# Kernel tuning notes

Measured on AMD Instinct MI355X. Metric: run time of the kernel, lower is better.

Reference implementation:

```python
import jax, jax.numpy as jnp
import numpy as np

HS = 256      # hidden_size
HD = 256      # hidden_dim
B, L, S = 256, 400, 512
N = B * L
E = N * 4
NEG_SLOPE = 0.2


def setup_inputs() -> dict:
    key = jax.random.key(0)
    ks = iter(jax.random.split(key, 48))
    def rn(shape, scale=0.05):
        return jax.random.normal(next(ks), shape, jnp.float32) * scale
    inp = {}
    inp['emb'] = jax.random.normal(next(ks), (N, 640), jnp.float32)
    inp['x_tokens'] = jax.random.randint(next(ks), (N,), 0, 6, jnp.int32)
    inp['edge_src'] = jax.random.randint(next(ks), (E,), 0, N, jnp.int32)
    inp['edge_dst'] = jax.random.randint(next(ks), (E,), 0, N, jnp.int32)
    inp['batch_ids'] = (jnp.arange(N, dtype=jnp.int32) // L)
    inp['pos_ids'] = (jnp.arange(N, dtype=jnp.int32) % L)
    inp['mask'] = (jnp.arange(S)[None, :] < L).astype(jnp.float32) * jnp.ones((B, 1), jnp.float32)
    # parameters
    inp['emb_table'] = rn((6, HS))
    inp['W_e2g'] = rn((640, HS)); inp['b_e2g'] = jnp.zeros((HS,), jnp.float32)
    # GAT layers: (in, heads*out), att_src/att_dst [heads, out], bias [out]
    inp['W1'] = rn((HS, 4 * HD)); inp['asrc1'] = rn((4, HD)); inp['adst1'] = rn((4, HD)); inp['b1'] = jnp.zeros((HD,), jnp.float32)
    inp['W2'] = rn((HD, 4 * HD)); inp['asrc2'] = rn((4, HD)); inp['adst2'] = rn((4, HD)); inp['b2'] = jnp.zeros((HD,), jnp.float32)
    inp['W3'] = rn((HD, 1 * HS)); inp['asrc3'] = rn((1, HS)); inp['adst3'] = rn((1, HS)); inp['b3'] = jnp.zeros((HS,), jnp.float32)
    inp['W_le'] = rn((640, HS)); inp['b_le'] = jnp.zeros((HS,), jnp.float32)
    # CNN conv kernels: OIH layout [out=128, in=256, k]
    inp['k7'] = rn((HS // 2, HS, 7)); inp['cb7'] = jnp.zeros((HS // 2,), jnp.float32)
    inp['k11'] = rn((HS // 2, HS, 11)); inp['cb11'] = jnp.zeros((HS // 2,), jnp.float32)
    inp['k15'] = rn((HS // 2, HS, 15)); inp['cb15'] = jnp.zeros((HS // 2,), jnp.float32)
    inp['Wl1'] = rn((HS // 2, 512)); inp['bl1'] = jnp.zeros((512,), jnp.float32)
    inp['Wl2'] = rn((512, HS)); inp['bl2'] = jnp.zeros((HS,), jnp.float32)
    return inp


def _gat(x, src, dst, W, a_src, a_dst, b, heads, out_dim):
    # PyG GATConv, concat=False, eval (no dropout), with self-loops.
    n = x.shape[0]
    h = (x @ W).reshape(n, heads, out_dim)             # [N,H,C]
    al_s = (h * a_src[None]).sum(-1)                   # [N,H]
    al_d = (h * a_dst[None]).sum(-1)                   # [N,H]
    e = al_s[src] + al_d[dst]                          # [E,H]
    e = jnp.where(e > 0, e, NEG_SLOPE * e)             # leaky_relu(0.2)
    m = jax.ops.segment_max(e, dst, num_segments=n)
    m = jnp.where(jnp.isfinite(m), m, 0.0)
    ex = jnp.exp(e - m[dst])
    denom = jax.ops.segment_sum(ex, dst, num_segments=n) + 1e-16
    alpha = ex / denom[dst]                            # [E,H]
    out = jax.ops.segment_sum(alpha[:, :, None] * h[src], dst, num_segments=n)
    return out.mean(axis=1) + b                        # concat=False -> mean over heads


def _conv1d(x, w, b, pad):
    # x: [B,C,S], w: [O,I,k]
    y = jax.lax.conv_general_dilated(x, w, (1,), [(pad, pad)],
                                     dimension_numbers=('NCH', 'OIH', 'NCH'))
    return y + b[None, :, None]


def reference(emb, x_tokens, edge_src, edge_dst, batch_ids, pos_ids, mask,
              emb_table, W_e2g, b_e2g,
              W1, asrc1, adst1, b1, W2, asrc2, adst2, b2, W3, asrc3, adst3, b3,
              W_le, b_le, k7, cb7, k11, cb11, k15, cb15, Wl1, bl1, Wl2, bl2):
    n = emb.shape[0]
    # self-loops (PyG GATConv default)
    loops = jnp.arange(n, dtype=edge_src.dtype)
    src = jnp.concatenate([edge_src, loops])
    dst = jnp.concatenate([edge_dst, loops])

    x_r = emb_table[x_tokens]                          # [N,HS]
    x_g = jax.nn.relu(emb @ W_e2g + b_e2g)             # [N,HS]
    x = jax.nn.relu(_gat(x_g, src, dst, W1, asrc1, adst1, b1, 4, HD))
    x = jax.nn.relu(_gat(x, src, dst, W2, asrc2, adst2, b2, 4, HD))
    x = jax.nn.relu(_gat(x, src, dst, W3, asrc3, adst3, b3, 1, HS))

    emb_l = jax.nn.relu(emb @ W_le + b_le)             # [N,HS]

    # ragged -> padded [B,S,HS] via scatter (vectorized form of the python loop)
    zeros = jnp.zeros((mask.shape[0], S, HS), jnp.float32)
    out_r = zeros.at[batch_ids, pos_ids].set((x_r + emb_l) / 2)

    # CNN (eval: dropout = identity)
    xc = out_r.transpose(0, 2, 1)                      # [B,HS,S]
    x1 = _conv1d(xc, k7, cb7, 3)
    x2 = _conv1d(xc, k11, cb11, 5)
    x3 = _conv1d(xc, k15, cb15, 7)
    xc = ((x1 + x2 + x3) / 3).transpose(0, 2, 1)       # [B,S,128]
    xc = jax.nn.relu(xc @ Wl1 + bl1) @ Wl2 + bl2       # [B,S,HS]

    emb_seq = (xc * mask[:, :, None]).mean(axis=1)     # [B,HS]
    return emb_seq
```

## Files before the change

### kernel.cpp

```cpp
#include <hip/hip_runtime.h>

#define NNODES 102400
#define NBATCH 256
#define LSEQ   400
#define SPAD   416
#define HS     256
#define KDIM   640
#define OC     128
#define NTAP   15
#define H1     512

typedef __attribute__((ext_vector_type(8))) short short8;
typedef __attribute__((ext_vector_type(4))) float floatx4;

__device__ inline unsigned short f2bf(float f) {
    unsigned u = __builtin_bit_cast(unsigned, f);
    unsigned r = (u + 0x7FFFu + ((u >> 16) & 1u)) >> 16;
    return (unsigned short)r;
}

__device__ inline void gld_lds16(const void* g, void* l) {
    __builtin_amdgcn_global_load_lds(
        (const __attribute__((address_space(1))) unsigned int*)g,
        (__attribute__((address_space(3))) unsigned int*)l, 16, 0, 0);
}

__global__ __launch_bounds__(256) void combine_pack(
    const float* __restrict__ k7, const float* __restrict__ k11,
    const float* __restrict__ k15, const float* __restrict__ cb7,
    const float* __restrict__ cb11, const float* __restrict__ cb15,
    unsigned short* __restrict__ Wpk, float* __restrict__ bc)
{
    int idx = blockIdx.x * 256 + threadIdx.x;
    if (idx < NTAP * HS * OC) {
        int oc = idx & (OC - 1);
        int ic = (idx >> 7) & (HS - 1);
        int d  = idx / (OC * HS);
        float w = k15[(oc * HS + ic) * 15 + d];
        int t11 = d - 2;
        if (t11 >= 0 && t11 < 11) w += k11[(oc * HS + ic) * 11 + t11];
        int t7 = d - 4;
        if (t7 >= 0 && t7 < 7)   w += k7[(oc * HS + ic) * 7 + t7];
        w *= (1.0f / 3.0f);
        int kc = ic >> 6, ks = (ic >> 5) & 1, q = (ic >> 3) & 3, j = ic & 7;
        int nt = oc >> 4, n = oc & 15;
        int pidx = ((((d * 4 + kc) * 2 + ks) * 8 + nt) * 64 + (q * 16 + n)) * 8 + j;
        Wpk[pidx] = f2bf(w);
    }
    if (idx < OC) bc[idx] = (cb7[idx] + cb11[idx] + cb15[idx]) * (1.0f / 3.0f);
}

__global__ __launch_bounds__(256) void pack_Wle(
    const float* __restrict__ W, unsigned short* __restrict__ P)
{
    int idx = blockIdx.x * 256 + threadIdx.x;
    int k = idx >> 8, col = idx & 255;
    int t = k >> 6, ks = (k >> 5) & 1, q = (k >> 3) & 3, j = k & 7;
    int nt = col >> 4, n = col & 15;
    int pidx = (((t * 2 + ks) * 16 + nt) * 64 + (q * 16 + n)) * 8 + j;
    P[pidx] = f2bf(W[k * 256 + col]);
}

__global__ __launch_bounds__(256) void pack_Wl1(
    const float* __restrict__ W, unsigned short* __restrict__ P)
{
    int idx = blockIdx.x * 256 + threadIdx.x;
    int k = idx >> 9, col = idx & 511;
    int ks = k >> 5, q = (k >> 3) & 3, j = k & 7;
    int jb = col >> 7, nhnt = (col >> 4) & 7, n = col & 15;
    int pidx = jb * 16384 + ((ks * 8 + nhnt) * 64 + (q * 16 + n)) * 8 + j;
    P[pidx] = f2bf(W[k * 512 + col]);
}

__global__ __launch_bounds__(256) void zero_pads(unsigned short* __restrict__ seq)
{
    int idx = blockIdx.x * 256 + threadIdx.x;
    int b = idx >> 9, within = idx & 511;
    int rowi = within >> 5, c = within & 31;
    int srow = rowi < 8 ? rowi : 400 + rowi;
    ((uint4*)seq)[((size_t)b * SPAD + srow) * 32 + c] = make_uint4(0u, 0u, 0u, 0u);
}

union GemmSm {
    struct { unsigned short As[64][72]; unsigned short Bsh[16384]; } s;
    unsigned short Cs[64][264];
};

__global__ __launch_bounds__(256) void gemm_emb(
    const float* __restrict__ emb, const int* __restrict__ x_tokens,
    const float* __restrict__ emb_table,
    const unsigned short* __restrict__ Wle_pk, const float* __restrict__ b_le,
    unsigned short* __restrict__ seq)
{
    __shared__ __align__(16) GemmSm g;
    int row0 = blockIdx.x * 64;
    int tid = threadIdx.x;
    int w = tid >> 6, lane = tid & 63;
    int q = lane >> 4, m = lane & 15;
    int mh = w >> 1, nh = w & 1;

    int ar = tid >> 2;
    int ac = (tid & 3) * 16;

    floatx4 acc[2][8] = {};
    const uint4* wp = (const uint4*)Wle_pk;

    for (int t = 0; t < 10; t++) {
        __syncthreads();
        {
            const float4* src = (const float4*)&emb[(size_t)(row0 + ar) * KDIM + t * 64 + ac];
            #pragma unroll
            for (int u = 0; u < 4; u++) {
                float4 f = src[u];
                ushort4 h;
                h.x = f2bf(f.x); h.y = f2bf(f.y); h.z = f2bf(f.z); h.w = f2bf(f.w);
                *(ushort4*)&g.s.As[ar][ac + u * 4] = h;
            }
        }
        #pragma unroll
        for (int i = 0; i < 8; i++) {
            gld_lds16(wp + (size_t)t * 2048 + i * 256 + tid,
                      &g.s.Bsh[(size_t)(i * 256 + w * 64) * 8]);
        }
        __syncthreads();

        #pragma unroll
        for (int ks = 0; ks < 2; ks++) {
            short8 a0 = *(const short8*)&g.s.As[mh * 32 + m][ks * 32 + q * 8];
            short8 a1 = *(const short8*)&g.s.As[mh * 32 + 16 + m][ks * 32 + q * 8];
            #pragma unroll
            for (int nt = 0; nt < 8; nt++) {
                short8 bf = *(const short8*)&g.s.Bsh[(size_t)((ks * 16 + nh * 8 + nt) * 64 + lane) * 8];
                acc[0][nt] = __builtin_amdgcn_mfma_f32_16x16x32_bf16(a0, bf, acc[0][nt], 0, 0, 0);
                acc[1][nt] = __builtin_amdgcn_mfma_f32_16x16x32_bf16(a1, bf, acc[1][nt], 0, 0, 0);
            }
        }
    }

    __syncthreads();
    #pragma unroll
    for (int nt = 0; nt < 8; nt++) {
        int col = nh * 128 + nt * 16 + m;
        float blv = b_le[col];
        #pragma unroll
        for (int mt = 0; mt < 2; mt++) {
            #pragma unroll
            for (int r = 0; r < 4; r++) {
                int row = mh * 32 + mt * 16 + q * 4 + r;
                int tok = x_tokens[row0 + row];
                float v = acc[mt][nt][r] + blv;
                v = v > 0.f ? v : 0.f;
                g.Cs[row][col] = f2bf(0.5f * (v + emb_table[tok * HS + col]));
            }
        }
    }
    __syncthreads();
    #pragma unroll
    for (int rr = 0; rr < 16; rr++) {
        int node = row0 + w * 16 + rr;
        int b = node / LSEQ;
        int p = node - b * LSEQ;
        ushort4 val = *(const ushort4*)&g.Cs[w * 16 + rr][lane * 4];
        *(ushort4*)&seq[((size_t)b * SPAD + (p + 8)) * HS + lane * 4] = val;
    }
}

union ConvSm {
    unsigned short As[78][264];
    float red[64 * 132];
};

__device__ __forceinline__ void conv_load_B(
    const short8* __restrict__ wb, int c, int kh, int nh, int lane, short8 bf[8])
{
    int d = c >> 1, kc = kh * 2 + (c & 1);
    const short8* bp = wb + (size_t)(d * 4 + kc) * 1024 + nh * 256 + lane;
    #pragma unroll
    for (int ks = 0; ks < 2; ks++)
        #pragma unroll
        for (int nt = 0; nt < 4; nt++)
            bf[ks * 4 + nt] = bp[(ks * 8 + nt) * 64];
}

__device__ __forceinline__ void conv_mfma_chunk(
    const unsigned short (*As)[264], floatx4 acc[4][4],
    const short8 bf[8], int c, int kh, int m, int q)
{
    int d = c >> 1, kc = kh * 2 + (c & 1);
    #pragma unroll
    for (int ks = 0; ks < 2; ks++) {
        #pragma unroll
        for (int mt = 0; mt < 4; mt++) {
            short8 a = *(const short8*)&As[mt * 16 + m + d][kc * 64 + ks * 32 + q * 8];
            #pragma unroll
            for (int nt = 0; nt < 4; nt++)
                acc[mt][nt] = __builtin_amdgcn_mfma_f32_16x16x32_bf16(a, bf[ks * 4 + nt], acc[mt][nt], 0, 0, 0);
        }
    }
}

__global__ __launch_bounds__(256, 3) void conv_mfma(
    const unsigned short* __restrict__ seq, const unsigned short* __restrict__ Wpk,
    const float* __restrict__ bc, unsigned short* __restrict__ convout)
{
    __shared__ __align__(16) ConvSm sm;

    int b  = blockIdx.y;
    int s0 = blockIdx.x * 64;
    int tid = threadIdx.x;
    int w = tid >> 6, lane = tid & 63;
    int q = lane >> 4, m = lane & 15;
    int nh = w >> 1, kh = w & 1;

    const short8* wb = (const short8*)Wpk;
    short8 bufA[8], bufB[8];
    conv_load_B(wb, 0, kh, nh, lane, bufA);

    {
        const uint4* sp = (const uint4*)(seq + ((size_t)b * SPAD + s0 + 1) * HS);
        #pragma unroll
        for (int pass = 0; pass < 10; pass++) {
            int idx = pass * 256 + tid;
            if (idx < 2496) {
                int r = idx >> 5, c = idx & 31;
                uint4 v = make_uint4(0u, 0u, 0u, 0u);
                if (s0 + 1 + r < SPAD) v = sp[r * 32 + c];
                *(uint4*)&sm.As[r][c * 8] = v;
            }
        }
    }
    __syncthreads();

    floatx4 acc[4][4] = {};

    for (int c = 0; c < 30; c += 2) {
        conv_load_B(wb, c + 1, kh, nh, lane, bufB);
        conv_mfma_chunk(sm.As, acc, bufA, c, kh, m, q);
        if (c + 2 < 30) conv_load_B(wb, c + 2, kh, nh, lane, bufA);
        conv_mfma_chunk(sm.As, acc, bufB, c + 1, kh, m, q);
    }

    __syncthreads();
    if (kh == 1) {
        #pragma unroll
        for (int mt = 0; mt < 4; mt++)
            #pragma unroll
            for (int nt = 0; nt < 4; nt++)
                #pragma unroll
                for (int r = 0; r < 4; r++)
                    sm.red[(mt * 16 + q * 4 + r) * 132 + nh * 64 + nt * 16 + m] = acc[mt][nt][r];
    }
    __syncthreads();
    if (kh == 0) {
        #pragma unroll
        for (int mt = 0; mt < 4; mt++)
            #pragma unroll
            for (int nt = 0; nt < 4; nt++)
                #pragma unroll
                for (int r = 0; r < 4; r++) {
                    int idx = (mt * 16 + q * 4 + r) * 132 + nh * 64 + nt * 16 + m;
                    sm.red[idx] += acc[mt][nt][r];
                }
    }
    __syncthreads();
    float b0 = bc[lane * 2], b1 = bc[lane * 2 + 1];
    #pragma unroll
    for (int rr = 0; rr < 16; rr++) {
        int row = w * 16 + rr;
        int s = s0 + row;
        if (s < LSEQ) {
            float2 v = *(const float2*)&sm.red[row * 132 + lane * 2];
            unsigned u = (unsigned)f2bf(v.x + b0) | ((unsigned)f2bf(v.y + b1) << 16);
            *(unsigned*)&convout[((size_t)b * LSEQ + s) * OC + lane * 2] = u;
        }
    }
}

__global__ __launch_bounds__(256) void mlp1_mfma(
    const unsigned short* __restrict__ convout, const unsigned short* __restrict__ Wl1_pk,
    const float* __restrict__ bl1, float* __restrict__ A_acc)
{
    __shared__ unsigned short As[64][136];
    __shared__ unsigned short Bsh[16384];
    int b  = blockIdx.z;
    int s0 = blockIdx.y * 64;
    int jb = blockIdx.x;
    int tid = threadIdx.x;
    int w = tid >> 6, lane = tid & 63;
    int q = lane >> 4, m = lane & 15;
    int mh = w >> 1, nh = w & 1;

    {
        int r = tid >> 2;
        int c = (tid & 3) * 32;
        const uint4* src = (const uint4*)&convout[((size_t)b * LSEQ + s0 + r) * OC + c];
        bool ok = (s0 + r) < LSEQ;
        #pragma unroll
        for (int u = 0; u < 4; u++) {
            uint4 v = make_uint4(0u, 0u, 0u, 0u);
            if (ok) v = src[u];
            *(uint4*)&As[r][c + u * 8] = v;
        }
    }
    {
        const uint4* wp = (const uint4*)(Wl1_pk + (size_t)jb * 16384);
        #pragma unroll
        for (int i = 0; i < 8; i++) {
            gld_lds16(wp + i * 256 + tid, &Bsh[(size_t)(i * 256 + w * 64) * 8]);
        }
    }
    __syncthreads();

    floatx4 acc[2][4] = {};
    #pragma unroll
    for (int ks = 0; ks < 4; ks++) {
        short8 a0 = *(const short8*)&As[mh * 32 + m][ks * 32 + q * 8];
        short8 a1 = *(const short8*)&As[mh * 32 + 16 + m][ks * 32 + q * 8];
        #pragma unroll
        for (int nt = 0; nt < 4; nt++) {
            short8 bf = *(const short8*)&Bsh[(size_t)((ks * 8 + nh * 4 + nt) * 64 + lane) * 8];
            acc[0][nt] = __builtin_amdgcn_mfma_f32_16x16x32_bf16(a0, bf, acc[0][nt], 0, 0, 0);
            acc[1][nt] = __builtin_amdgcn_mfma_f32_16x16x32_bf16(a1, bf, acc[1][nt], 0, 0, 0);
        }
    }

    #pragma unroll
    for (int nt = 0; nt < 4; nt++) {
        int j = jb * 128 + nh * 64 + nt * 16 + m;
        float blv = bl1[j];
        float vsum = 0.f;
        #pragma unroll
        for (int mt = 0; mt < 2; mt++) {
            int sbase = s0 + mh * 32 + mt * 16 + q * 4;
            #pragma unroll
            for (int r = 0; r < 4; r++) {
                if (sbase + r < LSEQ) {
                    float v = acc[mt][nt][r] + blv;
                    vsum += v > 0.f ? v : 0.f;
                }
            }
        }
        vsum += __shfl_xor(vsum, 16, 64);
        vsum += __shfl_xor(vsum, 32, 64);
        if (q == 0) atomicAdd(&A_acc[(size_t)b * H1 + j], vsum);
    }
}

__global__ __launch_bounds__(256) void final_out(
    const float* __restrict__ A_acc, const float* __restrict__ Wl2,
    const float* __restrict__ bl2, float* __restrict__ out)
{
    __shared__ float a[H1];
    int b = blockIdx.x, tid = threadIdx.x;
    a[tid] = A_acc[(size_t)b * H1 + tid];
    a[tid + 256] = A_acc[(size_t)b * H1 + tid + 256];
    __syncthreads();
    float acc = 0.f;
    #pragma unroll 8
    for (int k = 0; k < H1; k++)
        acc += a[k] * Wl2[(size_t)k * HS + tid];
    out[(size_t)b * HS + tid] = acc * (1.0f / 512.0f) + bl2[tid] * (400.0f / 512.0f);
}

extern "C" void kernel_launch(void* const* d_in, const int* in_sizes, int n_in,
                              void* d_out, int out_size, void* d_ws, size_t ws_size,
                              hipStream_t stream)
{
    const float* emb       = (const float*)d_in[0];
    const int*   x_tokens  = (const int*)d_in[1];
    const float* emb_table = (const float*)d_in[7];
    const float* W_le = (const float*)d_in[22];
    const float* b_le = (const float*)d_in[23];
    const float* k7   = (const float*)d_in[24];
    const float* cb7  = (const float*)d_in[25];
    const float* k11  = (const float*)d_in[26];
    const float* cb11 = (const float*)d_in[27];
    const float* k15  = (const float*)d_in[28];
    const float* cb15 = (const float*)d_in[29];
    const float* Wl1  = (const float*)d_in[30];
    const float* bl1  = (const float*)d_in[31];
    const float* Wl2  = (const float*)d_in[32];
    const float* bl2  = (const float*)d_in[33];
    float* out = (float*)d_out;

    char* p = (char*)d_ws;
    unsigned short* seqb = (unsigned short*)p;       p += (size_t)NBATCH * SPAD * HS * 2;
    unsigned short* convout = (unsigned short*)p;    p += (size_t)NBATCH * LSEQ * OC * 2;
    unsigned short* Wpk = (unsigned short*)p;        p += (size_t)NTAP * HS * OC * 2;
    unsigned short* Wle_pk = (unsigned short*)p;     p += (size_t)KDIM * HS * 2;
    unsigned short* Wl1_pk = (unsigned short*)p;     p += (size_t)OC * H1 * 2;
    float* bcv = (float*)p;                          p += 512;
    float* A_acc = (float*)p;                        p += (size_t)NBATCH * H1 * 4;

    hipMemsetAsync(A_acc, 0, (size_t)NBATCH * H1 * sizeof(float), stream);

    zero_pads<<<dim3(NBATCH * 512 / 256), 256, 0, stream>>>(seqb);
    combine_pack<<<dim3((NTAP * HS * OC + 255) / 256), 256, 0, stream>>>(
        k7, k11, k15, cb7, cb11, cb15, Wpk, bcv);
    pack_Wle<<<dim3(KDIM * HS / 256), 256, 0, stream>>>(W_le, Wle_pk);
    pack_Wl1<<<dim3(OC * H1 / 256), 256, 0, stream>>>(Wl1, Wl1_pk);
    gemm_emb<<<dim3(NNODES / 64), 256, 0, stream>>>(
        emb, x_tokens, emb_table, Wle_pk, b_le, seqb);
    conv_mfma<<<dim3(7, NBATCH), 256, 0, stream>>>(seqb, Wpk, bcv, convout);
    mlp1_mfma<<<dim3(4, 7, NBATCH), 256, 0, stream>>>(convout, Wl1_pk, bl1, A_acc);
    final_out<<<NBATCH, 256, 0, stream>>>(A_acc, Wl2, bl2, out);
}
```

Baseline: 679.4 us.

## Fuse conv and first MLP into one kernel, retile to 80 rows, merge setup kernels

The conv kernel now also runs the Wl1 GEMM, bias, ReLU and sequence-sum reduction straight from shared memory, so the bf16 convout intermediate no longer goes through global memory and the separate mlp1 launch is gone. The sequence tile grows from 64 to 80 rows, so the 400 positions split into 5 tiles with no tail masking. Launch bounds drop from 3 to 2 blocks per CU to fit the extra accumulators and shared memory. The four setup kernels and the memset are merged into one launch. The risks are lower occupancy and serialized per-jb weight loads inside the conv block.

```diff
diff --git a/kernel.cpp b/kernel.cpp
--- a/kernel.cpp
+++ b/kernel.cpp
@@ -9,6 +9,8 @@
 #define OC     128
 #define NTAP   15
 #define H1     512
+#define STILE  80
+#define SROWS  94
 
 typedef __attribute__((ext_vector_type(8))) short short8;
 typedef __attribute__((ext_vector_type(4))) float floatx4;
@@ -25,60 +27,56 @@
         (__attribute__((address_space(3))) unsigned int*)l, 16, 0, 0);
 }
 
-__global__ __launch_bounds__(256) void combine_pack(
+__global__ __launch_bounds__(256) void setup_all(
     const float* __restrict__ k7, const float* __restrict__ k11,
     const float* __restrict__ k15, const float* __restrict__ cb7,
     const float* __restrict__ cb11, const float* __restrict__ cb15,
-    unsigned short* __restrict__ Wpk, float* __restrict__ bc)
-{
-    int idx = blockIdx.x * 256 + threadIdx.x;
-    if (idx < NTAP * HS * OC) {
+    const float* __restrict__ W_le, const float* __restrict__ Wl1,
+    unsigned short* __restrict__ Wpk, float* __restrict__ bc,
+    unsigned short* __restrict__ Wle_pk, unsigned short* __restrict__ Wl1_pk,
+    unsigned short* __restrict__ seq, float* __restrict__ A_acc)
+{
+    int bid = blockIdx.x, tid = threadIdx.x;
+    if (bid < 512) {
+        int idx = bid * 256 + tid;
+        int b = idx >> 9, within = idx & 511;
+        int rowi = within >> 5, c = within & 31;
+        int srow = rowi < 8 ? rowi : 400 + rowi;
+        ((uint4*)seq)[((size_t)b * SPAD + srow) * 32 + c] = make_uint4(0u, 0u, 0u, 0u);
+    } else if (bid < 2432) {
+        int idx = (bid - 512) * 256 + tid;
         int oc = idx & (OC - 1);
         int ic = (idx >> 7) & (HS - 1);
         int d  = idx / (OC * HS);
-        float w = k15[(oc * HS + ic) * 15 + d];
+        float wv = k15[(oc * HS + ic) * 15 + d];
         int t11 = d - 2;
-        if (t11 >= 0 && t11 < 11) w += k11[(oc * HS + ic) * 11 + t11];
+        if (t11 >= 0 && t11 < 11) wv += k11[(oc * HS + ic) * 11 + t11];
         int t7 = d - 4;
-        if (t7 >= 0 && t7 < 7)   w += k7[(oc * HS + ic) * 7 + t7];
-        w *= (1.0f / 3.0f);
-        int kc = ic >> 6, ks = (ic >> 5) & 1, q = (ic >> 3) & 3, j = ic & 7;
+        if (t7 >= 0 && t7 < 7)   wv += k7[(oc * HS + ic) * 7 + t7];
+        wv *= (1.0f / 3.0f);
+        int kc = ic >> 6, ks = (ic >> 5) & 1, qq = (ic >> 3) & 3, j = ic & 7;
         int nt = oc >> 4, n = oc & 15;
-        int pidx = ((((d * 4 + kc) * 2 + ks) * 8 + nt) * 64 + (q * 16 + n)) * 8 + j;
-        Wpk[pidx] = f2bf(w);
-    }
-    if (idx < OC) bc[idx] = (cb7[idx] + cb11[idx] + cb15[idx]) * (1.0f / 3.0f);
-}
-
-__global__ __launch_bounds__(256) void pack_Wle(
-    const float* __restrict__ W, unsigned short* __restrict__ P)
-{
-    int idx = blockIdx.x * 256 + threadIdx.x;
-    int k = idx >> 8, col = idx & 255;
-    int t = k >> 6, ks = (k >> 5) & 1, q = (k >> 3) & 3, j = k & 7;
-    int nt = col >> 4, n = col & 15;
-    int pidx = (((t * 2 + ks) * 16 + nt) * 64 + (q * 16 + n)) * 8 + j;
-    P[pidx] = f2bf(W[k * 256 + col]);
-}
-
-__global__ __launch_bounds__(256) void pack_Wl1(
-    const float* __restrict__ W, unsigned short* __restrict__ P)
-{
-    int idx = blockIdx.x * 256 + threadIdx.x;
-    int k = idx >> 9, col = idx & 511;
-    int ks = k >> 5, q = (k >> 3) & 3, j = k & 7;
-    int jb = col >> 7, nhnt = (col >> 4) & 7, n = col & 15;
-    int pidx = jb * 16384 + ((ks * 8 + nhnt) * 64 + (q * 16 + n)) * 8 + j;
-    P[pidx] = f2bf(W[k * 512 + col]);
-}
-
-__global__ __launch_bounds__(256) void zero_pads(unsigned short* __restrict__ seq)
-{
-    int idx = blockIdx.x * 256 + threadIdx.x;
-    int b = idx >> 9, within = idx & 511;
-    int rowi = within >> 5, c = within & 31;
-    int srow = rowi < 8 ? rowi : 400 + rowi;
-    ((uint4*)seq)[((size_t)b * SPAD + srow) * 32 + c] = make_uint4(0u, 0u, 0u, 0u);
+        int pidx = ((((d * 4 + kc) * 2 + ks) * 8 + nt) * 64 + (qq * 16 + n)) * 8 + j;
+        Wpk[pidx] = f2bf(wv);
+        if (idx < OC) bc[idx] = (cb7[idx] + cb11[idx] + cb15[idx]) * (1.0f / 3.0f);
+    } else if (bid < 3072) {
+        int idx = (bid - 2432) * 256 + tid;
+        int k = idx >> 8, col = idx & 255;
+        int t = k >> 6, ks = (k >> 5) & 1, qq = (k >> 3) & 3, j = k & 7;
+        int nt = col >> 4, n = col & 15;
+        int pidx = (((t * 2 + ks) * 16 + nt) * 64 + (qq * 16 + n)) * 8 + j;
+        Wle_pk[pidx] = f2bf(W_le[k * 256 + col]);
+    } else if (bid < 3328) {
+        int idx = (bid - 3072) * 256 + tid;
+        int k = idx >> 9, col = idx & 511;
+        int ks = k >> 5, qq = (k >> 3) & 3, j = k & 7;
+        int jbb = col >> 7, nhnt = (col >> 4) & 7, n = col & 15;
+        int pidx = jbb * 16384 + ((ks * 8 + nhnt) * 64 + (qq * 16 + n)) * 8 + j;
+        Wl1_pk[pidx] = f2bf(Wl1[k * 512 + col]);
+    } else {
+        int idx = (bid - 3328) * 256 + tid;
+        ((float4*)A_acc)[idx] = make_float4(0.f, 0.f, 0.f, 0.f);
+    }
 }
 
 union GemmSm {
@@ -166,8 +164,14 @@
 }
 
 union ConvSm {
-    unsigned short As[78][264];
-    float red[64 * 132];
+    unsigned short As[SROWS][264];
+    struct {
+        union {
+            float red[STILE * 132];
+            unsigned short Bsh[16384];
+        } rb;
+        unsigned short abf[STILE][136];
+    } p2;
 };
 
 __device__ __forceinline__ void conv_load_B(
@@ -183,14 +187,14 @@
 }
 
 __device__ __forceinline__ void conv_mfma_chunk(
-    const unsigned short (*As)[264], floatx4 acc[4][4],
+    const unsigned short (*As)[264], floatx4 acc[5][4],
     const short8 bf[8], int c, int kh, int m, int q)
 {
     int d = c >> 1, kc = kh * 2 + (c & 1);
     #pragma unroll
     for (int ks = 0; ks < 2; ks++) {
         #pragma unroll
-        for (int mt = 0; mt < 4; mt++) {
+        for (int mt = 0; mt < 5; mt++) {
             short8 a = *(const short8*)&As[mt * 16 + m + d][kc * 64 + ks * 32 + q * 8];
             #pragma unroll
             for (int nt = 0; nt < 4; nt++)
@@ -199,14 +203,15 @@
     }
 }
 
-__global__ __launch_bounds__(256, 3) void conv_mfma(
+__global__ __launch_bounds__(256, 2) void conv_fused(
     const unsigned short* __restrict__ seq, const unsigned short* __restrict__ Wpk,
-    const float* __restrict__ bc, unsigned short* __restrict__ convout)
+    const float* __restrict__ bc, const unsigned short* __restrict__ Wl1_pk,
+    const float* __restrict__ bl1, float* __restrict__ A_acc)
 {
     __shared__ __align__(16) ConvSm sm;
 
     int b  = blockIdx.y;
-    int s0 = blockIdx.x * 64;
+    int s0 = blockIdx.x * STILE;
     int tid = threadIdx.x;
     int w = tid >> 6, lane = tid & 63;
     int q = lane >> 4, m = lane & 15;
@@ -219,19 +224,17 @@
     {
         const uint4* sp = (const uint4*)(seq + ((size_t)b * SPAD + s0 + 1) * HS);
         #pragma unroll
-        for (int pass = 0; pass < 10; pass++) {
+        for (int pass = 0; pass < 12; pass++) {
             int idx = pass * 256 + tid;
-            if (idx < 2496) {
+            if (idx < SROWS * 32) {
                 int r = idx >> 5, c = idx & 31;
-                uint4 v = make_uint4(0u, 0u, 0u, 0u);
-                if (s0 + 1 + r < SPAD) v = sp[r * 32 + c];
-                *(uint4*)&sm.As[r][c * 8] = v;
-            }
-        }
-    }
-    __syncthreads();
-
-    floatx4 acc[4][4] = {};
+                *(uint4*)&sm.As[r][c * 8] = sp[r * 32 + c];
+            }
+        }
+    }
+    __syncthreads();
+
+    floatx4 acc[5][4] = {};
 
     for (int c = 0; c < 30; c += 2) {
         conv_load_B(wb, c + 1, kh, nh, lane, bufB);
@@ -243,106 +246,74 @@
     __syncthreads();
     if (kh == 1) {
         #pragma unroll
-        for (int mt = 0; mt < 4; mt++)
+        for (int mt = 0; mt < 5; mt++)
             #pragma unroll
             for (int nt = 0; nt < 4; nt++)
                 #pragma unroll
                 for (int r = 0; r < 4; r++)
-                    sm.red[(mt * 16 + q * 4 + r) * 132 + nh * 64 + nt * 16 + m] = acc[mt][nt][r];
+                    sm.p2.rb.red[(mt * 16 + q * 4 + r) * 132 + nh * 64 + nt * 16 + m] = acc[mt][nt][r];
     }
     __syncthreads();
     if (kh == 0) {
         #pragma unroll
-        for (int mt = 0; mt < 4; mt++)
+        for (int mt = 0; mt < 5; mt++)
             #pragma unroll
             for (int nt = 0; nt < 4; nt++)
                 #pragma unroll
+                for (int r = 0; r < 4; r++)
+                    sm.p2.rb.red[(mt * 16 + q * 4 + r) * 132 + nh * 64 + nt * 16 + m] += acc[mt][nt][r];
+    }
+    __syncthreads();
+    {
+        float b0 = bc[lane * 2], b1 = bc[lane * 2 + 1];
+        #pragma unroll
+        for (int rr = 0; rr < 20; rr++) {
+            int row = w * 20 + rr;
+            float2 v = *(const float2*)&sm.p2.rb.red[row * 132 + lane * 2];
+            unsigned uo = (unsigned)f2bf(v.x + b0) | ((unsigned)f2bf(v.y + b1) << 16);
+            *(unsigned*)&sm.p2.abf[row][lane * 2] = uo;
+        }
+    }
+    __syncthreads();
+
+    for (int jb = 0; jb < 4; jb++) {
+        {
+            const uint4* wp = (const uint4*)(Wl1_pk + (size_t)jb * 16384);
+            #pragma unroll
+            for (int i = 0; i < 8; i++)
+                gld_lds16(wp + i * 256 + tid, &sm.p2.rb.Bsh[(size_t)(i * 256 + w * 64) * 8]);
+        }
+        __syncthreads();
+
+        floatx4 acc2[5][2] = {};
+        #pragma unroll
+        for (int ks = 0; ks < 4; ks++) {
+            short8 bf0 = *(const short8*)&sm.p2.rb.Bsh[(size_t)((ks * 8 + w * 2 + 0) * 64 + lane) * 8];
+            short8 bf1 = *(const short8*)&sm.p2.rb.Bsh[(size_t)((ks * 8 + w * 2 + 1) * 64 + lane) * 8];
+            #pragma unroll
+            for (int mt = 0; mt < 5; mt++) {
+                short8 a = *(const short8*)&sm.p2.abf[mt * 16 + m][ks * 32 + q * 8];
+                acc2[mt][0] = __builtin_amdgcn_mfma_f32_16x16x32_bf16(a, bf0, acc2[mt][0], 0, 0, 0);
+                acc2[mt][1] = __builtin_amdgcn_mfma_f32_16x16x32_bf16(a, bf1, acc2[mt][1], 0, 0, 0);
+            }
+        }
+        #pragma unroll
+        for (int nt = 0; nt < 2; nt++) {
+            int j = jb * 128 + w * 32 + nt * 16 + m;
+            float blv = bl1[j];
+            float vsum = 0.f;
+            #pragma unroll
+            for (int mt = 0; mt < 5; mt++)
+                #pragma unroll
                 for (int r = 0; r < 4; r++) {
-                    int idx = (mt * 16 + q * 4 + r) * 132 + nh * 64 + nt * 16 + m;
-                    sm.red[idx] += acc[mt][nt][r];
-                }
-    }
-    __syncthreads();
-    float b0 = bc[lane * 2], b1 = bc[lane * 2 + 1];
-    #pragma unroll
-    for (int rr = 0; rr < 16; rr++) {
-        int row = w * 16 + rr;
-        int s = s0 + row;
-        if (s < LSEQ) {
-            float2 v = *(const float2*)&sm.red[row * 132 + lane * 2];
-            unsigned u = (unsigned)f2bf(v.x + b0) | ((unsigned)f2bf(v.y + b1) << 16);
-            *(unsigned*)&convout[((size_t)b * LSEQ + s) * OC + lane * 2] = u;
-        }
-    }
-}
-
-__global__ __launch_bounds__(256) void mlp1_mfma(
-    const unsigned short* __restrict__ convout, const unsigned short* __restrict__ Wl1_pk,
-    const float* __restrict__ bl1, float* __restrict__ A_acc)
-{
-    __shared__ unsigned short As[64][136];
-    __shared__ unsigned short Bsh[16384];
-    int b  = blockIdx.z;
-    int s0 = blockIdx.y * 64;
-    int jb = blockIdx.x;
-    int tid = threadIdx.x;
-    int w = tid >> 6, lane = tid & 63;
-    int q = lane >> 4, m = lane & 15;
-    int mh = w >> 1, nh = w & 1;
-
-    {
-        int r = tid >> 2;
-        int c = (tid & 3) * 32;
-        const uint4* src = (const uint4*)&convout[((size_t)b * LSEQ + s0 + r) * OC + c];
-        bool ok = (s0 + r) < LSEQ;
-        #pragma unroll
-        for (int u = 0; u < 4; u++) {
-            uint4 v = make_uint4(0u, 0u, 0u, 0u);
-            if (ok) v = src[u];
-            *(uint4*)&As[r][c + u * 8] = v;
-        }
-    }
-    {
-        const uint4* wp = (const uint4*)(Wl1_pk + (size_t)jb * 16384);
-        #pragma unroll
-        for (int i = 0; i < 8; i++) {
-            gld_lds16(wp + i * 256 + tid, &Bsh[(size_t)(i * 256 + w * 64) * 8]);
-        }
-    }
-    __syncthreads();
-
-    floatx4 acc[2][4] = {};
-    #pragma unroll
-    for (int ks = 0; ks < 4; ks++) {
-        short8 a0 = *(const short8*)&As[mh * 32 + m][ks * 32 + q * 8];
-        short8 a1 = *(const short8*)&As[mh * 32 + 16 + m][ks * 32 + q * 8];
-        #pragma unroll
-        for (int nt = 0; nt < 4; nt++) {
-            short8 bf = *(const short8*)&Bsh[(size_t)((ks * 8 + nh * 4 + nt) * 64 + lane) * 8];
-            acc[0][nt] = __builtin_amdgcn_mfma_f32_16x16x32_bf16(a0, bf, acc[0][nt], 0, 0, 0);
-            acc[1][nt] = __builtin_amdgcn_mfma_f32_16x16x32_bf16(a1, bf, acc[1][nt], 0, 0, 0);
-        }
-    }
-
-    #pragma unroll
-    for (int nt = 0; nt < 4; nt++) {
-        int j = jb * 128 + nh * 64 + nt * 16 + m;
-        float blv = bl1[j];
-        float vsum = 0.f;
-        #pragma unroll
-        for (int mt = 0; mt < 2; mt++) {
-            int sbase = s0 + mh * 32 + mt * 16 + q * 4;
-            #pragma unroll
-            for (int r = 0; r < 4; r++) {
-                if (sbase + r < LSEQ) {
-                    float v = acc[mt][nt][r] + blv;
+                    float v = acc2[mt][nt][r] + blv;
                     vsum += v > 0.f ? v : 0.f;
                 }
-            }
-        }
-        vsum += __shfl_xor(vsum, 16, 64);
-        vsum += __shfl_xor(vsum, 32, 64);
-        if (q == 0) atomicAdd(&A_acc[(size_t)b * H1 + j], vsum);
+            vsum += __shfl_xor(vsum, 16, 64);
+            vsum += __shfl_xor(vsum, 32, 64);
+            if (q == 0) atomicAdd(&A_acc[(size_t)b * H1 + j], vsum);
+        }
+        __syncthreads();
     }
 }
 
@@ -385,23 +356,18 @@
 
     char* p = (char*)d_ws;
     unsigned short* seqb = (unsigned short*)p;       p += (size_t)NBATCH * SPAD * HS * 2;
-    unsigned short* convout = (unsigned short*)p;    p += (size_t)NBATCH * LSEQ * OC * 2;
     unsigned short* Wpk = (unsigned short*)p;        p += (size_t)NTAP * HS * OC * 2;
     unsigned short* Wle_pk = (unsigned short*)p;     p += (size_t)KDIM * HS * 2;
     unsigned short* Wl1_pk = (unsigned short*)p;     p += (size_t)OC * H1 * 2;
     float* bcv = (float*)p;                          p += 512;
     float* A_acc = (float*)p;                        p += (size_t)NBATCH * H1 * 4;
 
-    hipMemsetAsync(A_acc, 0, (size_t)NBATCH * H1 * sizeof(float), stream);
-
-    zero_pads<<<dim3(NBATCH * 512 / 256), 256, 0, stream>>>(seqb);
-    combine_pack<<<dim3((NTAP * HS * OC + 255) / 256), 256, 0, stream>>>(
-        k7, k11, k15, cb7, cb11, cb15, Wpk, bcv);
-    pack_Wle<<<dim3(KDIM * HS / 256), 256, 0, stream>>>(W_le, Wle_pk);
-    pack_Wl1<<<dim3(OC * H1 / 256), 256, 0, stream>>>(Wl1, Wl1_pk);
+    setup_all<<<dim3(3456), 256, 0, stream>>>(
+        k7, k11, k15, cb7, cb11, cb15, W_le, Wl1,
+        Wpk, bcv, Wle_pk, Wl1_pk, seqb, A_acc);
     gemm_emb<<<dim3(NNODES / 64), 256, 0, stream>>>(
         emb, x_tokens, emb_table, Wle_pk, b_le, seqb);
-    conv_mfma<<<dim3(7, NBATCH), 256, 0, stream>>>(seqb, Wpk, bcv, convout);
-    mlp1_mfma<<<dim3(4, 7, NBATCH), 256, 0, stream>>>(convout, Wl1_pk, bl1, A_acc);
+    conv_fused<<<dim3(5, NBATCH), 256, 0, stream>>>(
+        seqb, Wpk, bcv, Wl1_pk, bl1, A_acc);
     final_out<<<NBATCH, 256, 0, stream>>>(A_acc, Wl2, bl2, out);
 }
```

Measured after the change: 592.6 us. 1.15x faster.
